# Kernel tuning notes

Hardware: AMD Instinct MI355X
Metric: run time of the kernel (lower is better)

## Reference

```python
import jax, jax.numpy as jnp
import numpy as np

# static config (mirrors init_kwargs)
F_T, S = 8, 24            # video_shape = (F_T, S, S)
K, DIL = 3, 1             # kernel_size, dilation (same for all 3 axes)
HEADS, DHEAD, DIM = 8, 64, 512
INNER = HEADS * DHEAD
PAD = DIL * (K - 1)       # causal: pad 2 at the FRONT of each spatial axis
KJ = K ** 3               # 27 neighbors per query
N_VID = F_T * S * S       # 4608 video tokens


def causal_pad(t):
    # t: [B, D, F, S, S] -> pad front of f/h/w axes (torch F.pad (PAD*?,0) causal layout)
    return jnp.pad(t, ((0, 0), (0, 0), (PAD, 0), (PAD, 0), (PAD, 0)))


def unfold3d(t):
    # torch unfoldNd equivalent. t: [B, D, F+PAD, S+PAD, S+PAD]
    # returns [B, N_VID, KJ, D]; kernel offsets ordered (kf, kh, kw) w fastest,
    # matching torch unfold's channel-major / kernel-minor layout after the
    # rearrange 'b (d j) i -> b i j d'.
    sl = []
    for i in range(K):
        for j in range(K):
            for kk in range(K):
                sl.append(t[:, :, i * DIL:i * DIL + F_T,
                                  j * DIL:j * DIL + S,
                                  kk * DIL:kk * DIL + S])
    u = jnp.stack(sl, axis=2)                      # [B, D, KJ, F, S, S]
    B, D = t.shape[0], t.shape[1]
    u = u.reshape(B, D, KJ, N_VID)
    return jnp.transpose(u, (0, 3, 2, 1))          # [B, N_VID, KJ, D]


def make_mask():
    # True where the neighbor falls into zero padding (out-of-range / future under causal pad)
    ones = jnp.ones((1, 1, F_T, S, S), jnp.float32)
    u = unfold3d(causal_pad(ones))[0, :, :, 0]     # [N_VID, KJ]
    m = u == 0.0
    return jnp.pad(m, ((0, 0), (1, 0)), constant_values=False)  # bos col never masked


def stable_softmax(t, alpha=32.0 ** 2):
    t = t / alpha
    t = t - jax.lax.stop_gradient(jnp.max(t, axis=-1, keepdims=True))
    return jax.nn.softmax(t * alpha, axis=-1)


def setup_inputs() -> dict:
    key = jax.random.key(0)
    ks = jax.random.split(key, 9)
    return {
        "x": jax.random.normal(ks[0], (1, N_VID + 1, DIM), jnp.float32),
        "Wq": jax.random.normal(ks[1], (DIM, INNER), jnp.float32) * 0.02,
        "Wkv": jax.random.normal(ks[2], (DIM, 2 * INNER), jnp.float32) * 0.02,
        "W_th": jax.random.normal(ks[3], (HEADS, HEADS), jnp.float32) * 0.2,
        "Wout": jax.random.normal(ks[4], (INNER, DIM), jnp.float32) * 0.02,
        "bout": jax.random.normal(ks[5], (DIM,), jnp.float32) * 0.02,
        "ax1": jax.random.normal(ks[6], (K, HEADS), jnp.float32),
        "ax2": jax.random.normal(ks[7], (K, HEADS), jnp.float32),
        "ax3": jax.random.normal(ks[8], (K, HEADS), jnp.float32),
    }


def reference(x, Wq, Wkv, W_th, Wout, bout, ax1, ax2, ax3):
    b, n, _ = x.shape                       # b=1, n = 1 + N_VID (no extra padding)
    h, d = HEADS, DHEAD
    scale = d ** -0.5

    q = x @ Wq
    k, v = jnp.split(x @ Wkv, 2, axis=-1)

    def to_heads(t):  # 'b n (h d) -> (b h) n d'
        return t.reshape(b, n, h, d).transpose(0, 2, 1, 3).reshape(b * h, n, d)

    q, k, v = map(to_heads, (q, k, v))
    q = q[:, 1:] * scale                    # drop bos query
    k_bos, v_bos = k[:, :1], v[:, :1]       # [bh, 1, d]
    k, v = k[:, 1:], v[:, 1:]

    def to_vid(t):  # 'b (f h w) d -> b d f h w'
        return t.reshape(b * h, F_T, S, S, d).transpose(0, 4, 1, 2, 3)

    ku = unfold3d(causal_pad(to_vid(k)))    # [bh, N, KJ, d]
    vu = unfold3d(causal_pad(to_vid(v)))
    N = ku.shape[1]

    kb = jnp.broadcast_to(k_bos[:, :, None, :], (b * h, N, 1, d))
    vb = jnp.broadcast_to(v_bos[:, :, None, :], (b * h, N, 1, d))
    ku = jnp.concatenate([kb, ku], axis=2)  # [bh, N, KJ+1, d]
    vu = jnp.concatenate([vb, vu], axis=2)

    sim = jnp.einsum('bid,bijd->bij', q, ku)                 # [bh, N, KJ+1]

    # axial relative position bias over the 3x3x3 kernel, pad 0 for bos column
    rel = (ax1[:, None, None, :] + ax2[None, :, None, :] + ax3[None, None, :, :])
    rel = rel.reshape(KJ, h)                                 # [27, h]
    bias = jnp.pad(rel.T[:, None, :], ((0, 0), (0, 0), (1, 0)))  # [h, 1, KJ+1]

    sim = sim.reshape(b, h, N, KJ + 1) + bias[None]
    mask = make_mask()                                       # [N, KJ+1]
    sim = jnp.where(mask[None, None], -jnp.finfo(sim.dtype).max, sim)

    attn = stable_softmax(sim)                               # [b, h, N, KJ+1]
    attn = jnp.einsum('hg,bgij->bhij', W_th, attn)           # talking heads 1x1 conv

    out = jnp.einsum('bhij,bhijd->bhid', attn, vu.reshape(b, h, N, KJ + 1, d))
    out = jnp.concatenate([v_bos.reshape(b, h, 1, d), out], axis=2)  # re-attach bos value
    out = out.transpose(0, 2, 1, 3).reshape(b, n, h * d)     # '(b h) n d -> b n (h d)'
    return out @ Wout + bout
```

## Files before the change

### kernel.cpp

```cpp
#include <hip/hip_runtime.h>
#include <hip/hip_bf16.h>


constexpr int TFR   = 8;
constexpr int SDIM  = 24;
constexpr int NVID  = TFR * SDIM * SDIM;
constexpr int NTOK  = NVID + 1;
constexpr int NH    = 8;
constexpr int DM    = 512;
constexpr int NJ    = 28;

typedef __attribute__((ext_vector_type(8))) short bf16x8;
typedef __attribute__((ext_vector_type(8))) unsigned short ushort8;
typedef __attribute__((ext_vector_type(4))) float f32x4;

typedef const __attribute__((address_space(1))) unsigned int* gas_ptr;
typedef __attribute__((address_space(3))) unsigned int* las_ptr;

__device__ __forceinline__ float bf2f(unsigned short u) {
    return __uint_as_float((unsigned)u << 16);
}
__device__ __forceinline__ unsigned short f2bf(float f) {
    __hip_bfloat16 h = __float2bfloat16(f);
    return reinterpret_cast<unsigned short&>(h);
}

__global__ __launch_bounds__(256)
void prep_w(const float* __restrict__ Wq, const float* __restrict__ Wkv,
            const float* __restrict__ Wout, const float* __restrict__ x,
            __hip_bfloat16* __restrict__ Wqkvt, __hip_bfloat16* __restrict__ Woutt,
            __hip_bfloat16* __restrict__ xb)
{
    const int tid = threadIdx.x;
    int tb = blockIdx.x;

    if (tb >= 1024) {
        const size_t base = (size_t)(tb - 1024) * 2048 + (size_t)tid * 8;
        if (base < (size_t)NTOK * DM) {
            const float4 f0 = *(const float4*)(x + base);
            const float4 f1 = *(const float4*)(x + base + 4);
            unsigned short v[8] = { f2bf(f0.x), f2bf(f0.y), f2bf(f0.z), f2bf(f0.w),
                                    f2bf(f1.x), f2bf(f1.y), f2bf(f1.z), f2bf(f1.w) };
            *(ushort8*)(xb + base) = *(const ushort8*)v;
        }
        return;
    }

    __shared__ float t[32][33];
    const float* W; __hip_bfloat16* Wt; int Nd, tX, rowOff;
    if (tb < 256)      { W = Wq;   Wt = Wqkvt; Nd = 512;  tX = 16; rowOff = 0;   }
    else if (tb < 768) { tb -= 256; W = Wkv;  Wt = Wqkvt; Nd = 1024; tX = 32; rowOff = 512; }
    else               { tb -= 768; W = Wout; Wt = Woutt; Nd = 512;  tX = 16; rowOff = 0;   }
    const int n0 = (tb % tX) * 32, k0 = (tb / tX) * 32;
    const int r  = tid >> 3;
    const int c4 = (tid & 7) * 4;
    const float4 v = *(const float4*)(W + (size_t)(k0 + r) * Nd + n0 + c4);
    t[r][c4 + 0] = v.x; t[r][c4 + 1] = v.y; t[r][c4 + 2] = v.z; t[r][c4 + 3] = v.w;
    __syncthreads();
    #pragma unroll
    for (int j = 0; j < 4; ++j)
        Wt[(size_t)(rowOff + n0 + r) * 512 + k0 + c4 + j] = __float2bfloat16(t[c4 + j][r]);
}

__global__ __launch_bounds__(256)
void gemm_qkv(const __hip_bfloat16* __restrict__ Ab, const __hip_bfloat16* __restrict__ Bt,
              float* __restrict__ Cq, __hip_bfloat16* __restrict__ Ckv, int M)
{
    constexpr int BM = 128, BN = 128, BK = 64, K = 512;
    __shared__ __align__(16) short As[BM * BK];
    __shared__ __align__(16) short Bs[BN * BK];

    const int tid  = threadIdx.x;
    const int bid  = blockIdx.x;
    const int xcd  = bid & 7, pos = bid >> 3;
    const int L    = (xcd < 4) ? xcd * 56 + pos : 224 + (xcd - 4) * 55 + pos;
    const int m0   = (L / 12) * BM;
    const int n0   = (L % 12) * BN;

    const int lane = tid & 63;
    const int wave = tid >> 6;
    const int wm   = (wave >> 1) * 64;
    const int wn   = (wave & 1) * 64;
    const int col  = lane & 15;
    const int quad = lane >> 4;

    f32x4 acc[4][4] = {};

    for (int k0 = 0; k0 < K; k0 += BK) {
        #pragma unroll
        for (int it = 0; it < 4; ++it) {
            const int idx = it * 256 + tid;
            const int r   = idx >> 3;
            const int u   = (idx & 7) ^ (r & 7);
            const int gm  = (m0 + r < M) ? (m0 + r) : (M - 1);
            const __hip_bfloat16* gp = Ab + (size_t)gm * K + k0 + u * 8;
            __builtin_amdgcn_global_load_lds(
                (gas_ptr)gp, (las_ptr)&As[(it * 256 + wave * 64) * 8], 16, 0, 0);
        }
        #pragma unroll
        for (int it = 0; it < 4; ++it) {
            const int idx = it * 256 + tid;
            const int r   = idx >> 3;
            const int u   = (idx & 7) ^ (r & 7);
            const __hip_bfloat16* gp = Bt + (size_t)(n0 + r) * K + k0 + u * 8;
            __builtin_amdgcn_global_load_lds(
                (gas_ptr)gp, (las_ptr)&Bs[(it * 256 + wave * 64) * 8], 16, 0, 0);
        }
        __syncthreads();

        #pragma unroll
        for (int ks = 0; ks < 2; ++ks) {
            bf16x8 af[4], bfr[4];
            #pragma unroll
            for (int mt = 0; mt < 4; ++mt) {
                const int r = wm + mt * 16 + col;
                const int u = (ks * 4 + quad) ^ (r & 7);
                af[mt] = *(const bf16x8*)(&As[r * BK + u * 8]);
            }
            #pragma unroll
            for (int nt = 0; nt < 4; ++nt) {
                const int r = wn + nt * 16 + col;
                const int u = (ks * 4 + quad) ^ (r & 7);
                bfr[nt] = *(const bf16x8*)(&Bs[r * BK + u * 8]);
            }
            #pragma unroll
            for (int mt = 0; mt < 4; ++mt)
                #pragma unroll
                for (int nt = 0; nt < 4; ++nt)
                    acc[mt][nt] = __builtin_amdgcn_mfma_f32_16x16x32_bf16(
                        af[mt], bfr[nt], acc[mt][nt], 0, 0, 0);
        }
        __syncthreads();
    }

    const bool isQ = (n0 < 512);
    #pragma unroll
    for (int mt = 0; mt < 4; ++mt) {
        #pragma unroll
        for (int r = 0; r < 4; ++r) {
            const int row = m0 + wm + mt * 16 + quad * 4 + r;
            if (row >= M) continue;
            #pragma unroll
            for (int nt = 0; nt < 4; ++nt) {
                const int cg = n0 + wn + nt * 16 + col;
                const float v = acc[mt][nt][r];
                if (isQ) Cq[(size_t)row * 512 + cg] = v * 0.125f;
                else     Ckv[(size_t)row * 1024 + (cg - 512)] = __float2bfloat16(v);
            }
        }
    }
}

__global__ __launch_bounds__(256)
void gemm_out(const __hip_bfloat16* __restrict__ A, const __hip_bfloat16* __restrict__ Bt,
              float* __restrict__ C, int M, const float* __restrict__ bias)
{
    constexpr int BM = 64, BN = 64, BK = 64, K = 512;
    __shared__ __align__(16) short As[BM * BK];
    __shared__ __align__(16) short Bs[BN * BK];

    const int tid  = threadIdx.x;
    const int bid  = blockIdx.x;
    const int L    = (bid & 7) * 73 + (bid >> 3);
    const int m0   = (L >> 3) * BM;
    const int n0   = (L & 7) * BN;
    const int lane = tid & 63;
    const int wave = tid >> 6;
    const int wm   = (wave >> 1) * 32;
    const int wn   = (wave & 1) * 32;
    const int col  = lane & 15;
    const int quad = lane >> 4;

    f32x4 acc[2][2] = {};

    for (int k0 = 0; k0 < K; k0 += BK) {
        #pragma unroll
        for (int it = 0; it < 2; ++it) {
            const int idx = it * 256 + tid;
            const int r   = idx >> 3;
            const int u   = (idx & 7) ^ (r & 7);
            const int gm  = (m0 + r < M) ? (m0 + r) : (M - 1);
            const __hip_bfloat16* gp = A + (size_t)gm * K + k0 + u * 8;
            __builtin_amdgcn_global_load_lds(
                (gas_ptr)gp, (las_ptr)&As[(it * 256 + wave * 64) * 8], 16, 0, 0);
        }
        #pragma unroll
        for (int it = 0; it < 2; ++it) {
            const int idx = it * 256 + tid;
            const int r   = idx >> 3;
            const int u   = (idx & 7) ^ (r & 7);
            const __hip_bfloat16* gp = Bt + (size_t)(n0 + r) * K + k0 + u * 8;
            __builtin_amdgcn_global_load_lds(
                (gas_ptr)gp, (las_ptr)&Bs[(it * 256 + wave * 64) * 8], 16, 0, 0);
        }
        __syncthreads();

        #pragma unroll
        for (int ks = 0; ks < 2; ++ks) {
            bf16x8 af[2], bfr[2];
            #pragma unroll
            for (int mt = 0; mt < 2; ++mt) {
                const int r = wm + mt * 16 + col;
                const int u = (ks * 4 + quad) ^ (r & 7);
                af[mt] = *(const bf16x8*)(&As[r * BK + u * 8]);
            }
            #pragma unroll
            for (int nt = 0; nt < 2; ++nt) {
                const int r = wn + nt * 16 + col;
                const int u = (ks * 4 + quad) ^ (r & 7);
                bfr[nt] = *(const bf16x8*)(&Bs[r * BK + u * 8]);
            }
            #pragma unroll
            for (int mt = 0; mt < 2; ++mt)
                #pragma unroll
                for (int nt = 0; nt < 2; ++nt)
                    acc[mt][nt] = __builtin_amdgcn_mfma_f32_16x16x32_bf16(
                        af[mt], bfr[nt], acc[mt][nt], 0, 0, 0);
        }
        __syncthreads();
    }

    #pragma unroll
    for (int mt = 0; mt < 2; ++mt) {
        #pragma unroll
        for (int r = 0; r < 4; ++r) {
            const int row = m0 + wm + mt * 16 + quad * 4 + r;
            if (row >= M) continue;
            #pragma unroll
            for (int nt = 0; nt < 2; ++nt) {
                const int cg = n0 + wn + nt * 16 + col;
                C[(size_t)row * 512 + cg] = acc[mt][nt][r] + bias[cg];
            }
        }
    }
}

__global__ __launch_bounds__(256)
void attn_v2(const float* __restrict__ Q, const __hip_bfloat16* __restrict__ KVb,
             __hip_bfloat16* __restrict__ O,
             const float* __restrict__ W_th,
             const float* __restrict__ ax1, const float* __restrict__ ax2,
             const float* __restrict__ ax3)
{
    __shared__ float attn_s[4][NH * NJ];
    __shared__ float mixed_s[4][NH * NJ];

    const int tid  = threadIdx.x;
    const int wave = tid >> 6;
    const int lane = tid & 63;
    const int g    = lane >> 3;
    const int s    = lane & 7;
    const int bsw  = (blockIdx.x & 7) * (NVID / 4 / 8) + (blockIdx.x >> 3);
    const int i    = __builtin_amdgcn_readfirstlane(bsw * 4 + (tid >> 6));
    const int qrow = i + 1;

    const int t  = i / (SDIM * SDIM);
    const int rm = i % (SDIM * SDIM);
    const int y  = rm / SDIM;
    const int x  = rm % SDIM;

    float qf[8];
    {
        const float4 q0 = *(const float4*)(Q + (size_t)qrow * DM + lane * 8);
        const float4 q1 = *(const float4*)(Q + (size_t)qrow * DM + lane * 8 + 4);
        qf[0] = q0.x; qf[1] = q0.y; qf[2] = q0.z; qf[3] = q0.w;
        qf[4] = q1.x; qf[5] = q1.y; qf[6] = q1.z; qf[7] = q1.w;
    }
    float a1[3], a2[3], a3[3];
    #pragma unroll
    for (int d = 0; d < 3; ++d) {
        a1[d] = ax1[d * NH + g];
        a2[d] = ax2[d * NH + g];
        a3[d] = ax3[d * NH + g];
    }

    float sim[NJ];
    #pragma unroll
    for (int j = 0; j < NJ; ++j) {
        int row; bool valid; float bias;
        if (j == 0) { row = 0; valid = true; bias = 0.f; }
        else {
            const int jp = j - 1;
            const int di = jp / 9, dj = (jp / 3) % 3, dk = jp % 3;
            const int tt = t + di - 2, yy = y + dj - 2, xx = x + dk - 2;
            valid = (tt >= 0) && (yy >= 0) && (xx >= 0);
            row = 1 + tt * SDIM * SDIM + yy * SDIM + xx;
            bias = a1[di] + a2[dj] + a3[dk];
        }
        if (valid) {
            const ushort8 kv = *(const ushort8*)(KVb + (size_t)row * 1024 + lane * 8);
            float p = 0.f;
            #pragma unroll
            for (int e = 0; e < 8; ++e) p += bf2f(kv[e]) * qf[e];
            p += __shfl_xor(p, 1);
            p += __shfl_xor(p, 2);
            p += __shfl_xor(p, 4);
            sim[j] = p + bias;
        } else {
            sim[j] = -1e30f;
        }
    }

    float m = -1e30f;
    #pragma unroll
    for (int j = 0; j < NJ; ++j) m = fmaxf(m, sim[j]);
    float ssum = 0.f;
    #pragma unroll
    for (int j = 0; j < NJ; ++j) { sim[j] = __expf(sim[j] - m); ssum += sim[j]; }
    const float inv = 1.f / ssum;
    #pragma unroll
    for (int j = 0; j < NJ; ++j) sim[j] *= inv;

    if (s == 0) {
        #pragma unroll
        for (int u = 0; u < 7; ++u) {
            f32x4 v4 = { sim[4*u], sim[4*u+1], sim[4*u+2], sim[4*u+3] };
            *(f32x4*)(&attn_s[wave][g * NJ + 4 * u]) = v4;
        }
    }
    __syncthreads();

    if (tid < NH * NJ) {
        const int h = tid / NJ, j = tid % NJ;
        #pragma unroll
        for (int q = 0; q < 4; ++q) {
            float acc = 0.f;
            #pragma unroll
            for (int gg = 0; gg < NH; ++gg)
                acc += W_th[h * NH + gg] * attn_s[q][gg * NJ + j];
            mixed_s[q][h * NJ + j] = acc;
        }
    }
    __syncthreads();

    float acc8[8] = {};
    #pragma unroll
    for (int j = 0; j < NJ; ++j) {
        int row; bool valid;
        if (j == 0) { row = 0; valid = true; }
        else {
            const int jp = j - 1;
            const int di = jp / 9, dj = (jp / 3) % 3, dk = jp % 3;
            const int tt = t + di - 2, yy = y + dj - 2, xx = x + dk - 2;
            valid = (tt >= 0) && (yy >= 0) && (xx >= 0);
            row = 1 + tt * SDIM * SDIM + yy * SDIM + xx;
        }
        if (valid) {
            const ushort8 vv = *(const ushort8*)(KVb + (size_t)row * 1024 + 512 + lane * 8);
            const float w = mixed_s[wave][g * NJ + j];
            #pragma unroll
            for (int e = 0; e < 8; ++e) acc8[e] += w * bf2f(vv[e]);
        }
    }

    unsigned short o[8];
    #pragma unroll
    for (int e = 0; e < 8; ++e) o[e] = f2bf(acc8[e]);
    *(ushort8*)(O + (size_t)qrow * DM + lane * 8) = *(const ushort8*)o;

    if (i == 0) {
        const ushort8 vb = *(const ushort8*)(KVb + 512 + lane * 8);
        *(ushort8*)(O + lane * 8) = vb;
    }
}

extern "C" void kernel_launch(void* const* d_in, const int* in_sizes, int n_in,
                              void* d_out, int out_size, void* d_ws, size_t ws_size,
                              hipStream_t stream)
{
    const float* x    = (const float*)d_in[0];
    const float* Wq   = (const float*)d_in[1];
    const float* Wkv  = (const float*)d_in[2];
    const float* W_th = (const float*)d_in[3];
    const float* Wout = (const float*)d_in[4];
    const float* bout = (const float*)d_in[5];
    const float* ax1  = (const float*)d_in[6];
    const float* ax2  = (const float*)d_in[7];
    const float* ax3  = (const float*)d_in[8];
    float* out = (float*)d_out;

    char* p = (char*)d_ws;
    float* Qf = (float*)p;                       p += (size_t)NTOK * DM * 4;
    __hip_bfloat16* KVb   = (__hip_bfloat16*)p;  p += (size_t)NTOK * 2 * DM * 2;
    __hip_bfloat16* Ob    = (__hip_bfloat16*)p;  p += (size_t)NTOK * DM * 2;
    __hip_bfloat16* Wqkvt = (__hip_bfloat16*)p;  p += (size_t)3 * DM * DM * 2;
    __hip_bfloat16* Woutt = (__hip_bfloat16*)p;  p += (size_t)DM * DM * 2;
    __hip_bfloat16* xb    = (__hip_bfloat16*)p;  p += (size_t)NTOK * DM * 2;

    const dim3 blk(256);

    prep_w<<<2177, blk, 0, stream>>>(Wq, Wkv, Wout, x, Wqkvt, Woutt, xb);

    gemm_qkv<<<444, blk, 0, stream>>>(xb, Wqkvt, Qf, KVb, NTOK);

    attn_v2<<<dim3(NVID / 4), blk, 0, stream>>>(Qf, KVb, Ob, W_th, ax1, ax2, ax3);

    gemm_out<<<584, blk, 0, stream>>>(Ob, Woutt, out, NTOK, bout);
}
```

Baseline: 131.1 us.

## Stage shared K/V neighbor rows in LDS per 4-query block

```diff
diff --git a/kernel.cpp b/kernel.cpp
--- a/kernel.cpp
+++ b/kernel.cpp
@@ -9,6 +9,7 @@
 constexpr int NH    = 8;
 constexpr int DM    = 512;
 constexpr int NJ    = 28;
+constexpr int NUROW = 55;
 
 typedef __attribute__((ext_vector_type(8))) short bf16x8;
 typedef __attribute__((ext_vector_type(8))) unsigned short ushort8;
@@ -235,13 +236,15 @@
     }
 }
 
-__global__ __launch_bounds__(256)
-void attn_v2(const float* __restrict__ Q, const __hip_bfloat16* __restrict__ KVb,
+__global__ __launch_bounds__(256, 1)
+void attn_v3(const float* __restrict__ Q, const __hip_bfloat16* __restrict__ KVb,
              __hip_bfloat16* __restrict__ O,
              const float* __restrict__ W_th,
              const float* __restrict__ ax1, const float* __restrict__ ax2,
              const float* __restrict__ ax3)
 {
+    __shared__ __align__(16) short k_lds[NUROW * 512];
+    __shared__ __align__(16) short v_lds[NUROW * 512];
     __shared__ float attn_s[4][NH * NJ];
     __shared__ float mixed_s[4][NH * NJ];
 
@@ -251,13 +254,35 @@
     const int g    = lane >> 3;
     const int s    = lane & 7;
     const int bsw  = (blockIdx.x & 7) * (NVID / 4 / 8) + (blockIdx.x >> 3);
-    const int i    = __builtin_amdgcn_readfirstlane(bsw * 4 + (tid >> 6));
+    const int i0   = __builtin_amdgcn_readfirstlane(bsw * 4);
+    const int i    = i0 + wave;
     const int qrow = i + 1;
 
-    const int t  = i / (SDIM * SDIM);
-    const int rm = i % (SDIM * SDIM);
+    const int t  = i0 / (SDIM * SDIM);
+    const int rm = i0 % (SDIM * SDIM);
     const int y  = rm / SDIM;
-    const int x  = rm % SDIM;
+    const int x0 = rm % SDIM;
+
+    #pragma unroll
+    for (int p = 0; p < 14; ++p) {
+        const int rs = p * 4 + wave;
+        if (rs <= 54) {
+            int grow;
+            if (rs == 54) grow = 0;
+            else {
+                const int di = rs / 18, dj = (rs / 6) % 3, dx = rs % 6;
+                const int tt = t - 2 + di, yy = y - 2 + dj, xx = x0 - 2 + dx;
+                grow = (tt >= 0 && yy >= 0 && xx >= 0)
+                     ? 1 + tt * SDIM * SDIM + yy * SDIM + xx : 0;
+            }
+            __builtin_amdgcn_global_load_lds(
+                (gas_ptr)(KVb + (size_t)grow * 1024 + lane * 8),
+                (las_ptr)&k_lds[rs * 512], 16, 0, 0);
+            __builtin_amdgcn_global_load_lds(
+                (gas_ptr)(KVb + (size_t)grow * 1024 + 512 + lane * 8),
+                (las_ptr)&v_lds[rs * 512], 16, 0, 0);
+        }
+    }
 
     float qf[8];
     {
@@ -274,21 +299,23 @@
         a3[d] = ax3[d * NH + g];
     }
 
+    __syncthreads();
+
     float sim[NJ];
     #pragma unroll
     for (int j = 0; j < NJ; ++j) {
-        int row; bool valid; float bias;
-        if (j == 0) { row = 0; valid = true; bias = 0.f; }
+        int lidx; bool valid; float bias;
+        if (j == 0) { lidx = 54; valid = true; bias = 0.f; }
         else {
             const int jp = j - 1;
             const int di = jp / 9, dj = (jp / 3) % 3, dk = jp % 3;
-            const int tt = t + di - 2, yy = y + dj - 2, xx = x + dk - 2;
+            const int tt = t + di - 2, yy = y + dj - 2, xx = x0 + wave + dk - 2;
             valid = (tt >= 0) && (yy >= 0) && (xx >= 0);
-            row = 1 + tt * SDIM * SDIM + yy * SDIM + xx;
+            lidx = (di * 3 + dj) * 6 + wave + dk;
             bias = a1[di] + a2[dj] + a3[dk];
         }
         if (valid) {
-            const ushort8 kv = *(const ushort8*)(KVb + (size_t)row * 1024 + lane * 8);
+            const ushort8 kv = *(const ushort8*)(&k_lds[lidx * 512 + lane * 8]);
             float p = 0.f;
             #pragma unroll
             for (int e = 0; e < 8; ++e) p += bf2f(kv[e]) * qf[e];
@@ -336,17 +363,17 @@
     float acc8[8] = {};
     #pragma unroll
     for (int j = 0; j < NJ; ++j) {
-        int row; bool valid;
-        if (j == 0) { row = 0; valid = true; }
+        int lidx; bool valid;
+        if (j == 0) { lidx = 54; valid = true; }
         else {
             const int jp = j - 1;
             const int di = jp / 9, dj = (jp / 3) % 3, dk = jp % 3;
-            const int tt = t + di - 2, yy = y + dj - 2, xx = x + dk - 2;
+            const int tt = t + di - 2, yy = y + dj - 2, xx = x0 + wave + dk - 2;
             valid = (tt >= 0) && (yy >= 0) && (xx >= 0);
-            row = 1 + tt * SDIM * SDIM + yy * SDIM + xx;
+            lidx = (di * 3 + dj) * 6 + wave + dk;
         }
         if (valid) {
-            const ushort8 vv = *(const ushort8*)(KVb + (size_t)row * 1024 + 512 + lane * 8);
+            const ushort8 vv = *(const ushort8*)(&v_lds[lidx * 512 + lane * 8]);
             const float w = mixed_s[wave][g * NJ + j];
             #pragma unroll
             for (int e = 0; e < 8; ++e) acc8[e] += w * bf2f(vv[e]);
@@ -359,7 +386,7 @@
     *(ushort8*)(O + (size_t)qrow * DM + lane * 8) = *(const ushort8*)o;
 
     if (i == 0) {
-        const ushort8 vb = *(const ushort8*)(KVb + 512 + lane * 8);
+        const ushort8 vb = *(const ushort8*)(&v_lds[54 * 512 + lane * 8]);
         *(ushort8*)(O + lane * 8) = vb;
     }
 }
@@ -393,7 +420,7 @@
 
     gemm_qkv<<<444, blk, 0, stream>>>(xb, Wqkvt, Qf, KVb, NTOK);
 
-    attn_v2<<<dim3(NVID / 4), blk, 0, stream>>>(Qf, KVb, Ob, W_th, ax1, ax2, ax3);
+    attn_v3<<<dim3(NVID / 4), blk, 0, stream>>>(Qf, KVb, Ob, W_th, ax1, ax2, ax3);
 
     gemm_out<<<584, blk, 0, stream>>>(Ob, Woutt, out, NTOK, bout);
 }
```

Result: slower. 155.9 us (+18.9%).
